# Kernel tuning notes

Measured on AMD Instinct MI355X. Metric: run time of the kernel, lower is better.

The kernel has to match this reference:

```python
import jax, jax.numpy as jnp
import numpy as np

SAMPLING = 16   # VGG16 feature stride
POOL = 7        # adaptive max pool output size
KMAX = 5        # max bin window; valid for ROI feature extents <= 28 cells
NEG = jnp.float32(-1e30)


def _bin_bounds(s0, L, i):
    # torch AdaptiveMaxPool2d bin i over a length-L crop starting at s0:
    # [s0 + floor(i*L/P), s0 + ceil((i+1)*L/P))
    bs = s0 + (i * L) // POOL
    be = s0 + ((i + 1) * L + POOL - 1) // POOL
    return bs, be


def setup_inputs() -> dict:
    key = jax.random.key(0)
    ks = jax.random.split(key, 12)
    N, C, Hf, Wf = 1024, 512, 50, 84
    Himg, Wimg = Hf * SAMPLING, Wf * SAMPLING
    # post-ReLU VGG features -> non-negative
    featmap = jax.random.uniform(ks[0], (1, C, Hf, Wf), dtype=jnp.float32)
    # ROI boxes [x0, y0, x1, y1] in pixel coords, extents in [32, 448] px
    x0 = jax.random.randint(ks[1], (N,), 0, Wimg - 448)
    y0 = jax.random.randint(ks[2], (N,), 0, Himg - 448)
    w = jax.random.randint(ks[3], (N,), 32, 449)
    h = jax.random.randint(ks[4], (N,), 32, 449)
    roi = jnp.stack([x0, y0, x0 + w, y0 + h], axis=1).astype(jnp.int32)
    d = C * POOL * POOL  # 25088
    W1 = jax.random.normal(ks[5], (d, 4096), dtype=jnp.float32) * 0.01
    b1 = jnp.zeros((4096,), jnp.float32)
    W2 = jax.random.normal(ks[6], (4096, 4096), dtype=jnp.float32) * 0.01
    b2 = jnp.zeros((4096,), jnp.float32)
    Wc = jax.random.normal(ks[7], (4096, 3), dtype=jnp.float32) * 0.01
    bc = jnp.zeros((3,), jnp.float32)
    Wr = jax.random.normal(ks[8], (4096, 12), dtype=jnp.float32) * 0.01
    br = jnp.zeros((12,), jnp.float32)
    return {"featmap": featmap, "roi": roi, "W1": W1, "b1": b1, "W2": W2,
            "b2": b2, "Wc": Wc, "bc": bc, "Wr": Wr, "br": br}


def _roipool(featmap, roi):
    fm = featmap[0]                       # (C, Hf, Wf)
    C, Hf, Wf = fm.shape
    rf = roi // SAMPLING                  # floor, coords are non-negative
    x0, y0, x1, y1 = rf[:, 0], rf[:, 1], rf[:, 2], rf[:, 3]
    # width expand: if x1-x0 <= 1 -> grow right if in-bounds else grow left
    nw = (x1 - x0) <= 1
    x0n = jnp.where(nw & ~(x1 < Wf), x0 - 1, x0)
    x1n = jnp.where(nw & (x1 < Wf), x1 + 1, x1)
    nh = (y1 - y0) <= 1
    y0n = jnp.where(nh & ~(y1 < Hf), y0 - 1, y0)
    y1n = jnp.where(nh & (y1 < Hf), y1 + 1, y1)
    # python slice semantics clamp to array bounds
    xs, xe = jnp.clip(x0n, 0, Wf), jnp.clip(x1n, 0, Wf)
    ys, ye = jnp.clip(y0n, 0, Hf), jnp.clip(y1n, 0, Hf)
    Lx, Ly = xe - xs, ye - ys
    ar = jnp.arange(KMAX)
    rows = []
    for i in range(POOL):                 # fixed 7x7 bins
        hs, he = _bin_bounds(ys, Ly, i)
        h_idx = hs[:, None] + ar          # (N, K)
        h_ok = h_idx < he[:, None]
        h_idx = jnp.clip(h_idx, 0, Hf - 1)
        cols = []
        for j in range(POOL):
            ws_, we_ = _bin_bounds(xs, Lx, j)
            w_idx = ws_[:, None] + ar     # (N, K)
            w_ok = w_idx < we_[:, None]
            w_idx = jnp.clip(w_idx, 0, Wf - 1)
            patch = fm[:, h_idx[:, :, None], w_idx[:, None, :]]  # (C, N, K, K)
            m = h_ok[:, :, None] & w_ok[:, None, :]              # (N, K, K)
            patch = jnp.where(m[None], patch, NEG)
            cols.append(patch.max(axis=(2, 3)))                  # (C, N)
        rows.append(jnp.stack(cols, 0))   # (7, C, N)
    pool = jnp.stack(rows, 0)             # (7, 7, C, N)
    return pool.transpose(3, 2, 0, 1).reshape(roi.shape[0], -1)  # (N, C*49)


def reference(featmap, roi, W1, b1, W2, b2, Wc, bc, Wr, br):
    pooled = _roipool(featmap, roi)       # (N, 25088)
    h = (pooled @ W1 + b1) @ W2 + b2      # two Linears, no activation (as in source)
    output_cls = jax.nn.softmax(h @ Wc + bc, axis=1)
    output_reg = h @ Wr + br
    return output_cls, output_reg
```

## Files before the change

### kernel.cpp

```cpp
#include <hip/hip_runtime.h>
#include <hip/hip_bf16.h>
#include <cstdint>
#include <cstddef>

typedef __attribute__((ext_vector_type(4))) float f32x4;
typedef __attribute__((ext_vector_type(8))) short s16x8;

__device__ __forceinline__ unsigned short f2bf(float f) {
    union { float f; unsigned u; } v; v.f = f;
    unsigned u = v.u;
    u += 0x7fffu + ((u >> 16) & 1u);
    return (unsigned short)(u >> 16);
}
__device__ __forceinline__ float bf2f(unsigned short u) {
    union { unsigned u; float f; } v; v.u = ((unsigned)u) << 16; return v.f;
}
__device__ __forceinline__ float lo_f(unsigned v) {
    union { unsigned u; float f; } w; w.u = v << 16; return w.f;
}
__device__ __forceinline__ float hi_f(unsigned v) {
    union { unsigned u; float f; } w; w.u = v & 0xffff0000u; return w.f;
}


__global__ __launch_bounds__(256) void transpose_fm(
        const float* __restrict__ fm, unsigned short* __restrict__ fmT) {
    __shared__ float tile[32][33];
    int p0 = blockIdx.x * 32, c0 = blockIdx.y * 32;
    int tx = threadIdx.x, ty = threadIdx.y;
    #pragma unroll
    for (int yy = ty; yy < 32; yy += 8) {
        int p = p0 + tx;
        if (p < 4200) tile[yy][tx] = fm[(size_t)(c0 + yy) * 4200 + p];
    }
    __syncthreads();
    #pragma unroll
    for (int yy = ty; yy < 32; yy += 8) {
        int p = p0 + yy;
        if (p < 4200) fmT[(size_t)p * 512 + c0 + tx] = f2bf(tile[tx][yy]);
    }
}

#define PB(NH, NW) { \
    uint2 v[NH * NW]; \
    _Pragma("unroll") for (int r = 0; r < NH; ++r) \
        _Pragma("unroll") for (int s = 0; s < NW; ++s) \
            v[r * NW + s] = *(const uint2*)(base + ho[r] + wo[s]); \
    float a0 = lo_f(v[0].x), a1 = hi_f(v[0].x); \
    float a2 = lo_f(v[0].y), a3 = hi_f(v[0].y); \
    _Pragma("unroll") for (int q = 1; q < NH * NW; ++q) { \
        a0 = fmaxf(a0, lo_f(v[q].x)); a1 = fmaxf(a1, hi_f(v[q].x)); \
        a2 = fmaxf(a2, lo_f(v[q].y)); a3 = fmaxf(a3, hi_f(v[q].y)); } \
    m0 = a0; m1 = a1; m2 = a2; m3 = a3; } break;

__global__ __launch_bounds__(256) void pool4(
        const unsigned short* __restrict__ fmT, const int* __restrict__ roi,
        unsigned short* __restrict__ pooled) {
    const int n = blockIdx.x;
    __shared__ int hoff[7][5], woff[7][5], hcnt[7], wcnt[7];
    if (threadIdx.x == 0) {
        int x0 = roi[n*4+0] / 16, y0 = roi[n*4+1] / 16;
        int x1 = roi[n*4+2] / 16, y1 = roi[n*4+3] / 16;
        if (x1 - x0 <= 1) { if (x1 < 84) x1 += 1; else x0 -= 1; }
        if (y1 - y0 <= 1) { if (y1 < 50) y1 += 1; else y0 -= 1; }
        int xs = min(max(x0, 0), 84), xe = min(max(x1, 0), 84);
        int ys = min(max(y0, 0), 50), ye = min(max(y1, 0), 50);
        int Lx = xe - xs, Ly = ye - ys;
        #pragma unroll
        for (int i = 0; i < 7; ++i) {
            int b0 = ys + (i * Ly) / 7, b1 = ys + ((i + 1) * Ly + 6) / 7;
            int he = min(b1, b0 + 5);
            hcnt[i] = he - b0;
            int c0 = xs + (i * Lx) / 7, c1 = xs + ((i + 1) * Lx + 6) / 7;
            int we = min(c1, c0 + 5);
            wcnt[i] = we - c0;
            #pragma unroll
            for (int q = 0; q < 5; ++q) {
                hoff[i][q] = (b0 + q) * 43008;
                woff[i][q] = (c0 + q) * 512;
            }
        }
    }
    __syncthreads();
    const int t = threadIdx.x;
    const int g = t >> 7;
    const int c4 = (t & 127) * 4;
    const unsigned short* base = fmT + c4;
    unsigned short* orow = pooled + (size_t)n * 25088;
    for (int bp = 0; bp < 25; ++bp) {
        int bin = bp * 2 + g;
        if (bin < 49) {
            int bi = bin / 7, bj = bin - bi * 7;
            int ho[5], wo[5];
            #pragma unroll
            for (int q = 0; q < 5; ++q) { ho[q] = hoff[bi][q]; wo[q] = woff[bj][q]; }
            int nh = hcnt[bi], nw = wcnt[bj];
            float m0, m1, m2, m3;
            switch ((nh - 1) * 5 + (nw - 1)) {
                case  0: PB(1,1)  case  1: PB(1,2)  case  2: PB(1,3)
                case  3: PB(1,4)  case  4: PB(1,5)
                case  5: PB(2,1)  case  6: PB(2,2)  case  7: PB(2,3)
                case  8: PB(2,4)  case  9: PB(2,5)
                case 10: PB(3,1)  case 11: PB(3,2)  case 12: PB(3,3)
                case 13: PB(3,4)  case 14: PB(3,5)
                case 15: PB(4,1)  case 16: PB(4,2)  case 17: PB(4,3)
                case 18: PB(4,4)  case 19: PB(4,5)
                case 20: PB(5,1)  case 21: PB(5,2)  case 22: PB(5,3)
                case 23: PB(5,4)  case 24: PB(5,5)
                default: m0 = m1 = m2 = m3 = 0.f; break;
            }
            ushort4 o;
            o.x = f2bf(m0); o.y = f2bf(m1); o.z = f2bf(m2); o.w = f2bf(m3);
            *(ushort4*)(orow + bin * 512 + c4) = o;
        }
    }
}

__global__ __launch_bounds__(256) void prep_wcat(
        const float* __restrict__ Wc, const float* __restrict__ Wr,
        unsigned short* __restrict__ WcatT) {
    int idx = blockIdx.x * 256 + threadIdx.x;
    int i = idx >> 4, j = idx & 15;
    float v = (j < 3) ? Wc[i * 3 + j] : (j < 15) ? Wr[i * 12 + (j - 3)] : 0.f;
    WcatT[(size_t)j * 4096 + i] = f2bf(v);
}

__global__ __launch_bounds__(512) void skinny_mfma(
        const float* __restrict__ A, const unsigned short* __restrict__ BT,
        float* __restrict__ partial, int R, int kchunk) {
    const int t = threadIdx.x, lane = t & 63, wave = t >> 6;
    const int r0 = blockIdx.x * 128 + wave * 16;
    const int k0 = blockIdx.y * kchunk;
    const int lr = lane & 15, lks = lane >> 4;
    const int steps = kchunk >> 5;
    const float* ap = A + (size_t)(r0 + lr) * 4096 + k0 + lks * 8;
    const unsigned short* bp = BT + (size_t)lr * 4096 + k0 + lks * 8;
    f32x4 acc = {0.f, 0.f, 0.f, 0.f};
    for (int s = 0; s < steps; ++s) {
        float4 f0 = *(const float4*)(ap + s * 32);
        float4 f1 = *(const float4*)(ap + s * 32 + 4);
        s16x8 b = *(const s16x8*)(bp + s * 32);
        union { unsigned short us[8]; s16x8 v; } a;
        a.us[0] = f2bf(f0.x); a.us[1] = f2bf(f0.y);
        a.us[2] = f2bf(f0.z); a.us[3] = f2bf(f0.w);
        a.us[4] = f2bf(f1.x); a.us[5] = f2bf(f1.y);
        a.us[6] = f2bf(f1.z); a.us[7] = f2bf(f1.w);
        acc = __builtin_amdgcn_mfma_f32_16x16x32_bf16(a.v, b, acc, 0, 0, 0);
    }
    const int row = r0 + (lane >> 4) * 4;
    float* op = partial + ((size_t)blockIdx.y * R + row) * 16 + lr;
    #pragma unroll
    for (int q = 0; q < 4; ++q) op[q * 16] = acc[q];
}

__global__ __launch_bounds__(256) void reduce_wf(
        const float* __restrict__ partial1, const float* __restrict__ b2,
        const float* __restrict__ Wc, const float* __restrict__ Wr,
        const float* __restrict__ bc, const float* __restrict__ br,
        float* __restrict__ Wf16, unsigned short* __restrict__ WfT,
        float* __restrict__ bfv) {
    const int t = threadIdx.x;
    if (blockIdx.x < 256) {
        int idx = blockIdx.x * 256 + t;
        float s = 0.f;
        #pragma unroll
        for (int sp = 0; sp < 8; ++sp) s += partial1[sp * 65536 + idx];
        Wf16[idx] = s;
        int i = idx >> 4, j = idx & 15;
        WfT[(size_t)j * 4096 + i] = f2bf(s);
    } else {
        float acc[15];
        #pragma unroll
        for (int j = 0; j < 15; ++j) acc[j] = 0.f;
        for (int i = t; i < 4096; i += 256) {
            float bv = b2[i];
            #pragma unroll
            for (int j = 0; j < 15; ++j)
                acc[j] += bv * ((j < 3) ? Wc[i * 3 + j] : Wr[i * 12 + (j - 3)]);
        }
        const int lane = t & 63, wv = t >> 6;
        __shared__ float red[4][15];
        #pragma unroll
        for (int j = 0; j < 15; ++j) {
            float x = acc[j];
            #pragma unroll
            for (int off = 32; off >= 1; off >>= 1) x += __shfl_xor(x, off, 64);
            if (lane == 0) red[wv][j] = x;
        }
        __syncthreads();
        if (t < 15)
            bfv[t] = red[0][t] + red[1][t] + red[2][t] + red[3][t]
                   + ((t < 3) ? bc[t] : br[t - 3]);
    }
}

__global__ __launch_bounds__(256) void reduce_wbig(
        const float* __restrict__ partial2, const float* __restrict__ Wf16,
        const float* __restrict__ bfv, const float* __restrict__ b1,
        unsigned short* __restrict__ WbigT, float* __restrict__ bbig) {
    const int t = threadIdx.x;
    if (blockIdx.x < 98) {
        const int r = blockIdx.x * 256 + t;
        float sj[16];
        #pragma unroll
        for (int j = 0; j < 16; ++j) sj[j] = 0.f;
        #pragma unroll
        for (int sp = 0; sp < 2; ++sp) {
            const float4* pp = (const float4*)(partial2 + ((size_t)sp * 25088 + r) * 16);
            float4 a = pp[0], b = pp[1], c = pp[2], d = pp[3];
            sj[0] += a.x; sj[1] += a.y; sj[2]  += a.z; sj[3]  += a.w;
            sj[4] += b.x; sj[5] += b.y; sj[6]  += b.z; sj[7]  += b.w;
            sj[8] += c.x; sj[9] += c.y; sj[10] += c.z; sj[11] += c.w;
            sj[12] += d.x; sj[13] += d.y; sj[14] += d.z; sj[15] += d.w;
        }
        const int c = r / 49, bin = r - c * 49;
        const int p = bin * 512 + c;
        #pragma unroll
        for (int j = 0; j < 16; ++j)
            WbigT[(size_t)j * 25088 + p] = f2bf(sj[j]);
    } else {
        float acc[15];
        #pragma unroll
        for (int j = 0; j < 15; ++j) acc[j] = 0.f;
        for (int i = t; i < 4096; i += 256) {
            float bv = b1[i];
            #pragma unroll
            for (int j = 0; j < 15; ++j) acc[j] += bv * Wf16[i * 16 + j];
        }
        const int lane = t & 63, wv = t >> 6;
        __shared__ float red[4][15];
        #pragma unroll
        for (int j = 0; j < 15; ++j) {
            float x = acc[j];
            #pragma unroll
            for (int off = 32; off >= 1; off >>= 1) x += __shfl_xor(x, off, 64);
            if (lane == 0) red[wv][j] = x;
        }
        __syncthreads();
        if (t < 16) {
            float s = 0.f;
            if (t < 15)
                s = red[0][t] + red[1][t] + red[2][t] + red[3][t] + bfv[t];
            bbig[t] = s;
        }
    }
}

__global__ __launch_bounds__(256) void final_gemm(
        const unsigned short* __restrict__ pooled,
        const unsigned short* __restrict__ WbigT,
        float* __restrict__ partialG) {
    const int t = threadIdx.x, lane = t & 63, wave = t >> 6;
    const int m0 = blockIdx.x * 16, kz = blockIdx.y;
    const int lr = lane & 15, lks = lane >> 4;
    f32x4 acc = {0.f, 0.f, 0.f, 0.f};
    const unsigned short* arow = pooled + (size_t)(m0 + lr) * 25088 + kz * 3136 + lks * 8;
    const unsigned short* brow = WbigT + (size_t)lr * 25088 + kz * 3136 + lks * 8;
    for (int s = wave; s < 98; s += 4) {
        s16x8 a = *(const s16x8*)(arow + s * 32);
        s16x8 b = *(const s16x8*)(brow + s * 32);
        acc = __builtin_amdgcn_mfma_f32_16x16x32_bf16(a, b, acc, 0, 0, 0);
    }
    __shared__ float red[4][64][4];
    #pragma unroll
    for (int r = 0; r < 4; ++r) red[wave][lane][r] = acc[r];
    __syncthreads();
    if (wave == 0) {
        #pragma unroll
        for (int r = 0; r < 4; ++r) {
            float s = red[0][lane][r] + red[1][lane][r] + red[2][lane][r] + red[3][lane][r];
            int row = m0 + (lane >> 4) * 4 + r;
            partialG[((size_t)kz * 1024 + row) * 16 + (lane & 15)] = s;
        }
    }
}

__global__ __launch_bounds__(256) void finalize_kernel(
        const float* __restrict__ partialG, const float* __restrict__ bbig,
        float* __restrict__ out) {
    const int m = blockIdx.x * 256 + threadIdx.x;
    float v[15];
    #pragma unroll
    for (int j = 0; j < 15; ++j) v[j] = bbig[j];
    for (int kz = 0; kz < 8; ++kz) {
        const float* p = partialG + ((size_t)kz * 1024 + m) * 16;
        #pragma unroll
        for (int j = 0; j < 15; ++j) v[j] += p[j];
    }
    float mx = fmaxf(v[0], fmaxf(v[1], v[2]));
    float e0 = expf(v[0] - mx), e1 = expf(v[1] - mx), e2 = expf(v[2] - mx);
    float inv = 1.f / (e0 + e1 + e2);
    out[m * 3 + 0] = e0 * inv;
    out[m * 3 + 1] = e1 * inv;
    out[m * 3 + 2] = e2 * inv;
    #pragma unroll
    for (int j = 3; j < 15; ++j) out[3072 + m * 12 + (j - 3)] = v[j];
}

extern "C" void kernel_launch(void* const* d_in, const int* in_sizes, int n_in,
                              void* d_out, int out_size, void* d_ws, size_t ws_size,
                              hipStream_t stream) {
    const float* featmap = (const float*)d_in[0];
    const int*   roi     = (const int*)d_in[1];
    const float* W1      = (const float*)d_in[2];
    const float* b1      = (const float*)d_in[3];
    const float* W2      = (const float*)d_in[4];
    const float* b2      = (const float*)d_in[5];
    const float* Wc      = (const float*)d_in[6];
    const float* bc      = (const float*)d_in[7];
    const float* Wr      = (const float*)d_in[8];
    const float* br      = (const float*)d_in[9];
    float* out = (float*)d_out;

    char* ws = (char*)d_ws;
    unsigned short* pooled   = (unsigned short*)(ws);
    unsigned short* fmT      = (unsigned short*)(ws + 51380224);
    unsigned short* WcatT    = (unsigned short*)(ws + 55681024);
    unsigned short* WfT      = (unsigned short*)(ws + 55812096);
    float*          Wf16     = (float*)        (ws + 55943168);
    float*          bfv      = (float*)        (ws + 56205312);
    float*          bbig     = (float*)        (ws + 56205376);
    float*          partial1 = (float*)        (ws + 56205440);
    float*          partial2 = (float*)        (ws + 60399744);
    unsigned short* WbigT    = (unsigned short*)(ws + 63611008);
    float*          partialG = (float*)        (ws + 64413824);

    transpose_fm<<<dim3(132, 16), dim3(32, 8), 0, stream>>>(featmap, fmT);
    pool4<<<1024, 256, 0, stream>>>(fmT, roi, pooled);
    prep_wcat<<<256, 256, 0, stream>>>(Wc, Wr, WcatT);
    skinny_mfma<<<dim3(32, 8), 512, 0, stream>>>(W2, WcatT, partial1, 4096, 512);
    reduce_wf<<<257, 256, 0, stream>>>(partial1, b2, Wc, Wr, bc, br, Wf16, WfT, bfv);
    skinny_mfma<<<dim3(196, 2), 512, 0, stream>>>(W1, WfT, partial2, 25088, 2048);
    reduce_wbig<<<99, 256, 0, stream>>>(partial2, Wf16, bfv, b1, WbigT, bbig);
    final_gemm<<<dim3(64, 8), 256, 0, stream>>>(pooled, WbigT, partialG);
    finalize_kernel<<<4, 256, 0, stream>>>(partialG, bbig, out);
}
```

Measured before the change: 228.1 us.

## Fuse ROI pooling with W1 skinny GEMM and merge prep kernels

Merges the featmap transpose and Wc/Wr packing into one launch. ROI pooling and the W1×Wf skinny MFMA now share a single interleaved kernel, so memory-bound gather work and bandwidth-heavy streaming of W1 overlap on the GPU. The W1 K-split goes from 2 to 4 chunks to create more blocks, which means reduce_wbig sums 4 partials and the workspace offsets shift. Pooling blocks now use 512 threads covering 4 bins per step. The cost is a larger partial buffer and mixed block shapes in one grid.

```diff
diff --git a/kernel.cpp b/kernel.cpp
--- a/kernel.cpp
+++ b/kernel.cpp
@@ -12,9 +12,6 @@
     u += 0x7fffu + ((u >> 16) & 1u);
     return (unsigned short)(u >> 16);
 }
-__device__ __forceinline__ float bf2f(unsigned short u) {
-    union { unsigned u; float f; } v; v.u = ((unsigned)u) << 16; return v.f;
-}
 __device__ __forceinline__ float lo_f(unsigned v) {
     union { unsigned u; float f; } w; w.u = v << 16; return w.f;
 }
@@ -23,114 +20,41 @@
 }
 
 
-__global__ __launch_bounds__(256) void transpose_fm(
-        const float* __restrict__ fm, unsigned short* __restrict__ fmT) {
-    __shared__ float tile[32][33];
-    int p0 = blockIdx.x * 32, c0 = blockIdx.y * 32;
-    int tx = threadIdx.x, ty = threadIdx.y;
-    #pragma unroll
-    for (int yy = ty; yy < 32; yy += 8) {
-        int p = p0 + tx;
-        if (p < 4200) tile[yy][tx] = fm[(size_t)(c0 + yy) * 4200 + p];
-    }
-    __syncthreads();
-    #pragma unroll
-    for (int yy = ty; yy < 32; yy += 8) {
-        int p = p0 + yy;
-        if (p < 4200) fmT[(size_t)p * 512 + c0 + tx] = f2bf(tile[tx][yy]);
-    }
-}
-
-#define PB(NH, NW) { \
-    uint2 v[NH * NW]; \
-    _Pragma("unroll") for (int r = 0; r < NH; ++r) \
-        _Pragma("unroll") for (int s = 0; s < NW; ++s) \
-            v[r * NW + s] = *(const uint2*)(base + ho[r] + wo[s]); \
-    float a0 = lo_f(v[0].x), a1 = hi_f(v[0].x); \
-    float a2 = lo_f(v[0].y), a3 = hi_f(v[0].y); \
-    _Pragma("unroll") for (int q = 1; q < NH * NW; ++q) { \
-        a0 = fmaxf(a0, lo_f(v[q].x)); a1 = fmaxf(a1, hi_f(v[q].x)); \
-        a2 = fmaxf(a2, lo_f(v[q].y)); a3 = fmaxf(a3, hi_f(v[q].y)); } \
-    m0 = a0; m1 = a1; m2 = a2; m3 = a3; } break;
-
-__global__ __launch_bounds__(256) void pool4(
-        const unsigned short* __restrict__ fmT, const int* __restrict__ roi,
-        unsigned short* __restrict__ pooled) {
-    const int n = blockIdx.x;
-    __shared__ int hoff[7][5], woff[7][5], hcnt[7], wcnt[7];
-    if (threadIdx.x == 0) {
-        int x0 = roi[n*4+0] / 16, y0 = roi[n*4+1] / 16;
-        int x1 = roi[n*4+2] / 16, y1 = roi[n*4+3] / 16;
-        if (x1 - x0 <= 1) { if (x1 < 84) x1 += 1; else x0 -= 1; }
-        if (y1 - y0 <= 1) { if (y1 < 50) y1 += 1; else y0 -= 1; }
-        int xs = min(max(x0, 0), 84), xe = min(max(x1, 0), 84);
-        int ys = min(max(y0, 0), 50), ye = min(max(y1, 0), 50);
-        int Lx = xe - xs, Ly = ye - ys;
-        #pragma unroll
-        for (int i = 0; i < 7; ++i) {
-            int b0 = ys + (i * Ly) / 7, b1 = ys + ((i + 1) * Ly + 6) / 7;
-            int he = min(b1, b0 + 5);
-            hcnt[i] = he - b0;
-            int c0 = xs + (i * Lx) / 7, c1 = xs + ((i + 1) * Lx + 6) / 7;
-            int we = min(c1, c0 + 5);
-            wcnt[i] = we - c0;
-            #pragma unroll
-            for (int q = 0; q < 5; ++q) {
-                hoff[i][q] = (b0 + q) * 43008;
-                woff[i][q] = (c0 + q) * 512;
-            }
-        }
-    }
-    __syncthreads();
-    const int t = threadIdx.x;
-    const int g = t >> 7;
-    const int c4 = (t & 127) * 4;
-    const unsigned short* base = fmT + c4;
-    unsigned short* orow = pooled + (size_t)n * 25088;
-    for (int bp = 0; bp < 25; ++bp) {
-        int bin = bp * 2 + g;
-        if (bin < 49) {
-            int bi = bin / 7, bj = bin - bi * 7;
-            int ho[5], wo[5];
-            #pragma unroll
-            for (int q = 0; q < 5; ++q) { ho[q] = hoff[bi][q]; wo[q] = woff[bj][q]; }
-            int nh = hcnt[bi], nw = wcnt[bj];
-            float m0, m1, m2, m3;
-            switch ((nh - 1) * 5 + (nw - 1)) {
-                case  0: PB(1,1)  case  1: PB(1,2)  case  2: PB(1,3)
-                case  3: PB(1,4)  case  4: PB(1,5)
-                case  5: PB(2,1)  case  6: PB(2,2)  case  7: PB(2,3)
-                case  8: PB(2,4)  case  9: PB(2,5)
-                case 10: PB(3,1)  case 11: PB(3,2)  case 12: PB(3,3)
-                case 13: PB(3,4)  case 14: PB(3,5)
-                case 15: PB(4,1)  case 16: PB(4,2)  case 17: PB(4,3)
-                case 18: PB(4,4)  case 19: PB(4,5)
-                case 20: PB(5,1)  case 21: PB(5,2)  case 22: PB(5,3)
-                case 23: PB(5,4)  case 24: PB(5,5)
-                default: m0 = m1 = m2 = m3 = 0.f; break;
-            }
-            ushort4 o;
-            o.x = f2bf(m0); o.y = f2bf(m1); o.z = f2bf(m2); o.w = f2bf(m3);
-            *(ushort4*)(orow + bin * 512 + c4) = o;
-        }
-    }
-}
-
-__global__ __launch_bounds__(256) void prep_wcat(
+__global__ __launch_bounds__(256) void prep_all(
+        const float* __restrict__ fm, unsigned short* __restrict__ fmT,
         const float* __restrict__ Wc, const float* __restrict__ Wr,
         unsigned short* __restrict__ WcatT) {
-    int idx = blockIdx.x * 256 + threadIdx.x;
-    int i = idx >> 4, j = idx & 15;
-    float v = (j < 3) ? Wc[i * 3 + j] : (j < 15) ? Wr[i * 12 + (j - 3)] : 0.f;
-    WcatT[(size_t)j * 4096 + i] = f2bf(v);
-}
-
-__global__ __launch_bounds__(512) void skinny_mfma(
+    const int bid = blockIdx.x, t = threadIdx.x;
+    if (bid < 2112) {
+        __shared__ float tile[32][33];
+        int p0 = (bid % 132) * 32, c0 = (bid / 132) * 32;
+        int tx = t & 31, ty = t >> 5;
+        #pragma unroll
+        for (int yy = ty; yy < 32; yy += 8) {
+            int p = p0 + tx;
+            if (p < 4200) tile[yy][tx] = fm[(size_t)(c0 + yy) * 4200 + p];
+        }
+        __syncthreads();
+        #pragma unroll
+        for (int yy = ty; yy < 32; yy += 8) {
+            int p = p0 + yy;
+            if (p < 4200) fmT[(size_t)p * 512 + c0 + tx] = f2bf(tile[tx][yy]);
+        }
+    } else {
+        int idx = (bid - 2112) * 256 + t;
+        int i = idx >> 4, j = idx & 15;
+        float v = (j < 3) ? Wc[i * 3 + j] : (j < 15) ? Wr[i * 12 + (j - 3)] : 0.f;
+        WcatT[(size_t)j * 4096 + i] = f2bf(v);
+    }
+}
+
+__device__ __forceinline__ void skinny_body(
         const float* __restrict__ A, const unsigned short* __restrict__ BT,
-        float* __restrict__ partial, int R, int kchunk) {
-    const int t = threadIdx.x, lane = t & 63, wave = t >> 6;
-    const int r0 = blockIdx.x * 128 + wave * 16;
-    const int k0 = blockIdx.y * kchunk;
+        float* __restrict__ partial, int R, int kchunk,
+        int bx, int ky, int t) {
+    const int lane = t & 63, wave = t >> 6;
+    const int r0 = bx * 128 + wave * 16;
+    const int k0 = ky * kchunk;
     const int lr = lane & 15, lks = lane >> 4;
     const int steps = kchunk >> 5;
     const float* ap = A + (size_t)(r0 + lr) * 4096 + k0 + lks * 8;
@@ -148,9 +72,15 @@
         acc = __builtin_amdgcn_mfma_f32_16x16x32_bf16(a.v, b, acc, 0, 0, 0);
     }
     const int row = r0 + (lane >> 4) * 4;
-    float* op = partial + ((size_t)blockIdx.y * R + row) * 16 + lr;
+    float* op = partial + ((size_t)ky * R + row) * 16 + lr;
     #pragma unroll
     for (int q = 0; q < 4; ++q) op[q * 16] = acc[q];
+}
+
+__global__ __launch_bounds__(512) void skinny_w2(
+        const float* __restrict__ W2, const unsigned short* __restrict__ WcatT,
+        float* __restrict__ partial1) {
+    skinny_body(W2, WcatT, partial1, 4096, 512, blockIdx.x, blockIdx.y, threadIdx.x);
 }
 
 __global__ __launch_bounds__(256) void reduce_wf(
@@ -194,6 +124,90 @@
     }
 }
 
+#define PB(NH, NW) { \
+    uint2 v[NH * NW]; \
+    _Pragma("unroll") for (int r = 0; r < NH; ++r) \
+        _Pragma("unroll") for (int s = 0; s < NW; ++s) \
+            v[r * NW + s] = *(const uint2*)(base + ho[r] + wo[s]); \
+    float a0 = lo_f(v[0].x), a1 = hi_f(v[0].x); \
+    float a2 = lo_f(v[0].y), a3 = hi_f(v[0].y); \
+    _Pragma("unroll") for (int q = 1; q < NH * NW; ++q) { \
+        a0 = fmaxf(a0, lo_f(v[q].x)); a1 = fmaxf(a1, hi_f(v[q].x)); \
+        a2 = fmaxf(a2, lo_f(v[q].y)); a3 = fmaxf(a3, hi_f(v[q].y)); } \
+    m0 = a0; m1 = a1; m2 = a2; m3 = a3; } break;
+
+__global__ __launch_bounds__(512) void megaB(
+        const unsigned short* __restrict__ fmT, const int* __restrict__ roi,
+        unsigned short* __restrict__ pooled,
+        const float* __restrict__ W1, const unsigned short* __restrict__ WfT,
+        float* __restrict__ partial2) {
+    const int g7 = blockIdx.x / 7, r7 = blockIdx.x % 7;
+    const int t = threadIdx.x;
+    if (r7 < 3) {
+        const int sb = g7 * 3 + r7;
+        if (sb >= 784) return;
+        const int ky = sb / 196, bx = sb % 196;
+        skinny_body(W1, WfT, partial2, 25088, 1024, bx, ky, t);
+    } else {
+        const int n = g7 * 4 + (r7 - 3);
+        if (n >= 1024) return;
+        __shared__ int hoff[7][5], woff[7][5], hcnt[7], wcnt[7];
+        if (t == 0) {
+            int x0 = roi[n*4+0] / 16, y0 = roi[n*4+1] / 16;
+            int x1 = roi[n*4+2] / 16, y1 = roi[n*4+3] / 16;
+            if (x1 - x0 <= 1) { if (x1 < 84) x1 += 1; else x0 -= 1; }
+            if (y1 - y0 <= 1) { if (y1 < 50) y1 += 1; else y0 -= 1; }
+            int xs = min(max(x0, 0), 84), xe = min(max(x1, 0), 84);
+            int ys = min(max(y0, 0), 50), ye = min(max(y1, 0), 50);
+            int Lx = xe - xs, Ly = ye - ys;
+            #pragma unroll
+            for (int i = 0; i < 7; ++i) {
+                int b0 = ys + (i * Ly) / 7, b1 = ys + ((i + 1) * Ly + 6) / 7;
+                hcnt[i] = min(b1, b0 + 5) - b0;
+                int c0 = xs + (i * Lx) / 7, c1 = xs + ((i + 1) * Lx + 6) / 7;
+                wcnt[i] = min(c1, c0 + 5) - c0;
+                #pragma unroll
+                for (int q = 0; q < 5; ++q) {
+                    hoff[i][q] = (b0 + q) * 43008;
+                    woff[i][q] = (c0 + q) * 512;
+                }
+            }
+        }
+        __syncthreads();
+        const int g = t >> 7;
+        const int c4 = (t & 127) * 4;
+        const unsigned short* base = fmT + c4;
+        unsigned short* orow = pooled + (size_t)n * 25088;
+        for (int bp = 0; bp < 13; ++bp) {
+            int bin = bp * 4 + g;
+            if (bin < 49) {
+                int bi = bin / 7, bj = bin - bi * 7;
+                int ho[5], wo[5];
+                #pragma unroll
+                for (int q = 0; q < 5; ++q) { ho[q] = hoff[bi][q]; wo[q] = woff[bj][q]; }
+                int nh = hcnt[bi], nw = wcnt[bj];
+                float m0, m1, m2, m3;
+                switch ((nh - 1) * 5 + (nw - 1)) {
+                    case  0: PB(1,1)  case  1: PB(1,2)  case  2: PB(1,3)
+                    case  3: PB(1,4)  case  4: PB(1,5)
+                    case  5: PB(2,1)  case  6: PB(2,2)  case  7: PB(2,3)
+                    case  8: PB(2,4)  case  9: PB(2,5)
+                    case 10: PB(3,1)  case 11: PB(3,2)  case 12: PB(3,3)
+                    case 13: PB(3,4)  case 14: PB(3,5)
+                    case 15: PB(4,1)  case 16: PB(4,2)  case 17: PB(4,3)
+                    case 18: PB(4,4)  case 19: PB(4,5)
+                    case 20: PB(5,1)  case 21: PB(5,2)  case 22: PB(5,3)
+                    case 23: PB(5,4)  case 24: PB(5,5)
+                    default: m0 = m1 = m2 = m3 = 0.f; break;
+                }
+                ushort4 o;
+                o.x = f2bf(m0); o.y = f2bf(m1); o.z = f2bf(m2); o.w = f2bf(m3);
+                *(ushort4*)(orow + bin * 512 + c4) = o;
+            }
+        }
+    }
+}
+
 __global__ __launch_bounds__(256) void reduce_wbig(
         const float* __restrict__ partial2, const float* __restrict__ Wf16,
         const float* __restrict__ bfv, const float* __restrict__ b1,
@@ -205,7 +219,7 @@
         #pragma unroll
         for (int j = 0; j < 16; ++j) sj[j] = 0.f;
         #pragma unroll
-        for (int sp = 0; sp < 2; ++sp) {
+        for (int sp = 0; sp < 4; ++sp) {
             const float4* pp = (const float4*)(partial2 + ((size_t)sp * 25088 + r) * 16);
             float4 a = pp[0], b = pp[1], c = pp[2], d = pp[3];
             sj[0] += a.x; sj[1] += a.y; sj[2]  += a.z; sj[3]  += a.w;
@@ -322,15 +336,13 @@
     float*          bbig     = (float*)        (ws + 56205376);
     float*          partial1 = (float*)        (ws + 56205440);
     float*          partial2 = (float*)        (ws + 60399744);
-    unsigned short* WbigT    = (unsigned short*)(ws + 63611008);
-    float*          partialG = (float*)        (ws + 64413824);
-
-    transpose_fm<<<dim3(132, 16), dim3(32, 8), 0, stream>>>(featmap, fmT);
-    pool4<<<1024, 256, 0, stream>>>(fmT, roi, pooled);
-    prep_wcat<<<256, 256, 0, stream>>>(Wc, Wr, WcatT);
-    skinny_mfma<<<dim3(32, 8), 512, 0, stream>>>(W2, WcatT, partial1, 4096, 512);
+    unsigned short* WbigT    = (unsigned short*)(ws + 66822272);
+    float*          partialG = (float*)        (ws + 67625088);
+
+    prep_all<<<2368, 256, 0, stream>>>(featmap, fmT, Wc, Wr, WcatT);
+    skinny_w2<<<dim3(32, 8), 512, 0, stream>>>(W2, WcatT, partial1);
     reduce_wf<<<257, 256, 0, stream>>>(partial1, b2, Wc, Wr, bc, br, Wf16, WfT, bfv);
-    skinny_mfma<<<dim3(196, 2), 512, 0, stream>>>(W1, WfT, partial2, 25088, 2048);
+    megaB<<<1834, 512, 0, stream>>>(fmT, roi, pooled, W1, WfT, partial2);
     reduce_wbig<<<99, 256, 0, stream>>>(partial2, Wf16, bfv, b1, WbigT, bbig);
     final_gemm<<<dim3(64, 8), 256, 0, stream>>>(pooled, WbigT, partialG);
     finalize_kernel<<<4, 256, 0, stream>>>(partialG, bbig, out);
```

After: 214.1 us. 1.07x faster.
